# Optimization experiments

Hardware: AMD Instinct MI355X
Metric: run time of the kernel (lower is better)

Reference implementation:

```python
import jax, jax.numpy as jnp
import numpy as np
from math import factorial

# ---- static config (mirrors CACE_LR defaults) ----
MAX_L, MAX_NU = 3, 3
N_RBF, N_RADIAL = 6, 6
N_BASIS = 3                       # n_atom_basis
N_CH = N_BASIS * N_BASIS          # edge channels = 9
CUTOFF, P = 5.5, 6
NZ = 94                           # elements with Z < 95
N_NODES, N_EDGES, N_GRAPHS = 10000, 80000, 16
MP_NORM = 1.0 / np.sqrt(10.0)     # 1/sqrt(avg_num_neighbors)

# Cartesian angular monomials x^lx y^ly z^lz with lx+ly+lz = l <= MAX_L
LXLYLZ = [(lx, ly, l - lx - ly) for l in range(MAX_L + 1)
          for lx in range(l, -1, -1) for ly in range(l - lx, -1, -1)]
N_ANG = len(LXLYLZ)               # 20
MONO = np.array(LXLYLZ, np.int32)
L_OF = MONO.sum(1)                # l of each monomial
IDX000 = LXLYLZ.index((0, 0, 0))
MIDX = {m: i for i, m in enumerate(LXLYLZ)}

def _mult(m):
    return factorial(sum(m)) / (factorial(m[0]) * factorial(m[1]) * factorial(m[2]))

MULT = np.array([_mult(m) for m in LXLYLZ], np.float32)
# nu=2 invariants: per l>=1, sum_m mult(m) * A_m^2
NU2_W = [np.where(L_OF == l, MULT, 0.0).astype(np.float32) for l in range(1, MAX_L + 1)]
# nu=3 invariants: pairs (l1,l2), contract A_m1 * A_m2 * A_{m1+m2}
NU3 = []
for (l1, l2) in [(1, 1), (1, 2)]:
    i1s, i2s, i12s, cfs = [], [], [], []
    for m1 in [m for m in LXLYLZ if sum(m) == l1]:
        for m2 in [m for m in LXLYLZ if sum(m) == l2]:
            m12 = (m1[0] + m2[0], m1[1] + m2[1], m1[2] + m2[2])
            i1s.append(MIDX[m1]); i2s.append(MIDX[m2]); i12s.append(MIDX[m12])
            cfs.append(_mult(m12))
    NU3.append((np.array(i1s), np.array(i2s), np.array(i12s), np.array(cfs, np.float32)))
N_SYM = 1 + MAX_L + len(NU3)      # 6 symmetrized angular features
FLAT_DIM = N_RADIAL * N_SYM * N_CH * 2  # 648


def monomials(u):                 # u: [E,3] unit vectors -> [E, N_ANG]
    pows = jnp.stack([jnp.ones_like(u), u, u * u, u * u * u], axis=1)  # [E,4,3]
    return pows[:, MONO[:, 0], 0] * pows[:, MONO[:, 1], 1] * pows[:, MONO[:, 2], 2]


def symmetrize(A):                # A: [N,R,N_ANG,C] -> B: [N,R,N_SYM,C]
    outs = [A[:, :, IDX000, :]]
    A2 = A * A
    for w in NU2_W:
        outs.append(jnp.einsum('nrac,a->nrc', A2, jnp.asarray(w)))
    for i1, i2, i12, cf in NU3:
        outs.append(jnp.einsum('nrkc,k->nrc', A[:, :, i1] * A[:, :, i2] * A[:, :, i12],
                               jnp.asarray(cf)))
    return jnp.stack(outs, axis=2)


def radial_tf(A, W):              # shared-per-l radial linear, W: [MAX_L+1,R,S]
    return jnp.einsum('nrac,ars->nsac', A, W[L_OF])


def setup_inputs() -> dict:
    key = jax.random.key(0)
    ks = jax.random.split(key, 16)
    pos = jax.random.uniform(ks[0], (N_NODES, 3), jnp.float32) * 10.0  # 10 A box
    node_type = jax.random.randint(ks[1], (N_NODES,), 0, NZ)
    src = jax.random.randint(ks[2], (N_EDGES,), 0, N_NODES)
    dst = jax.random.randint(ks[3], (N_EDGES,), 0, N_NODES)
    shifts = jnp.zeros((N_EDGES, 3), jnp.float32)
    batch_ids = jnp.sort(jax.random.randint(ks[4], (N_NODES,), 0, N_GRAPHS))
    s = lambda k, sh, f: jax.random.normal(k, sh, jnp.float32) * f
    params = dict(
        Wemb=s(ks[5], (NZ, N_BASIS), 0.5),
        freqs=jnp.arange(1, N_RBF + 1, dtype=jnp.float32) * np.pi / CUTOFF,
        W_rt=s(ks[6], (MAX_L + 1, N_RBF, N_RADIAL), 1 / np.sqrt(N_RBF)),
        W_mem=s(ks[7], (MAX_L + 1, N_RADIAL, N_RADIAL), 1 / np.sqrt(N_RADIAL)),
        W_Ar=s(ks[8], (MAX_L + 1, N_RBF, N_RADIAL), 1 / np.sqrt(N_RBF)),
        W_chi=s(ks[9], (N_RADIAL * N_SYM * N_CH, N_CH), 1 / np.sqrt(N_RADIAL * N_SYM * N_CH)),
        W1=s(ks[10], (FLAT_DIM, 64), 1 / np.sqrt(FLAT_DIM)),
        b1=jnp.zeros((64,), jnp.float32),
        W2=s(ks[11], (64, 32), 1 / 8.0),
        b2=jnp.zeros((32,), jnp.float32),
        W3=s(ks[12], (32, 1), 1 / np.sqrt(32.0)),
        b3=jnp.zeros((1,), jnp.float32),
    )
    return dict(pos=pos, node_type=node_type, src=src, dst=dst,
                shifts=shifts, batch_ids=batch_ids, **params)


def reference(pos, node_type, src, dst, shifts, batch_ids, Wemb, freqs,
              W_rt, W_mem, W_Ar, W_chi, W1, b1, W2, b2, W3, b3):
    n = pos.shape[0]
    # edge geometry (get_edge_vectors_and_lengths, normalize=True)
    vec = pos[dst] - pos[src] + shifts
    r = jnp.linalg.norm(vec, axis=-1, keepdims=True) + 1e-9           # [E,1]
    unit = vec / r
    # Bessel RBF and polynomial cutoff (p=6)
    rbf = jnp.sqrt(2.0 / CUTOFF) * jnp.sin(r * freqs[None]) / r      # [E,R]
    u = r[:, 0] / CUTOFF
    fc = jnp.where(u < 1.0,
                   1.0 - (P + 1) * (P + 2) / 2.0 * u**P + P * (P + 2) * u**(P + 1)
                   - P * (P + 1) / 2.0 * u**(P + 2), 0.0)
    radial = rbf * fc[:, None]
    ang = monomials(unit)                                             # [E,N_ANG]
    # node one-hot + embedding folded into a table lookup; directed edge encoding
    emb = Wemb[node_type]                                             # [N,3]
    edge_code = (emb[src][:, :, None] * emb[dst][:, None, :]).reshape(-1, N_CH)
    # edge_attri[e,r,a,c] = radial * angular * edge_code
    edge_attri = radial[:, :, None, None] * ang[:, None, :, None] * edge_code[:, None, None, :]
    A = radial_tf(jax.ops.segment_sum(edge_attri, dst, num_segments=n), W_rt)
    B = symmetrize(A)
    B_list = [B]
    # ---- one message-passing step: M (memory) + Ar + Bchi ----
    memory = radial_tf(A, W_mem)
    chi = B.reshape(n, -1) @ W_chi                                    # [N,C]
    msg_B = edge_attri * chi[src][:, None, None, :]
    A_B = radial_tf(jax.ops.segment_sum(msg_B, dst, num_segments=n), W_rt)
    rad_Ar = jnp.einsum('er,ars->eas', rbf, W_Ar[L_OF]) * fc[:, None, None]  # [E,A,S]
    msg_Ar = A[src] * jnp.transpose(rad_Ar, (0, 2, 1))[:, :, :, None]
    A_r = jax.ops.segment_sum(msg_Ar, dst, num_segments=n)
    A = (A_r + A_B) * MP_NORM + memory
    B_list.append(symmetrize(A))
    feats = jnp.stack(B_list, axis=-1).reshape(n, -1)                 # [N, 648]
    # MLP readout (atomwise_hidden=[64,32], num_targets=1), SiLU activations
    h = jax.nn.silu(feats @ W1 + b1)
    h = jax.nn.silu(h @ W2 + b2)
    atomic = h @ W3 + b3                                              # [N,1]
    return jnp.squeeze(jax.ops.segment_sum(atomic, batch_ids, num_segments=N_GRAPHS))
```

## Files before the change

kernel.cpp:

```cpp
#include <hip/hip_runtime.h>
#include <hip/hip_bf16.h>
#include <math.h>

#define NE 80000
#define NN 10000
#define NG 16
#define NBLK 157
#define MP_NORM 0.31622776601683794f
#define RBF_NORM 0.60302268915552724f

__constant__ int c_mx[20] = {0, 1,0,0, 2,1,1,0,0,0, 3,2,2,1,1,1,0,0,0,0};
__constant__ int c_my[20] = {0, 0,1,0, 0,1,0,2,1,0, 0,1,0,2,1,0,3,2,1,0};
__constant__ int c_mz[20] = {0, 0,0,1, 0,0,1,0,1,2, 0,0,1,0,1,2,0,1,2,3};

__device__ __forceinline__ int l_of_a(int a) {
    return (a >= 10) ? 3 : ((a >= 4) ? 2 : ((a >= 1) ? 1 : 0));
}

__device__ __forceinline__ void symm_from_lds(const float* Als, float* brow,
                                              int lane) {
    if (lane >= 54) return;
    const int s2 = lane / 9, c = lane - s2 * 9;
    const float* a = Als + s2 * 180 + c;
    float v[20];
    #pragma unroll
    for (int i = 0; i < 20; i++) v[i] = a[i * 9];
    const float o0 = v[0];
    const float o1 = v[1]*v[1] + v[2]*v[2] + v[3]*v[3];
    const float o2 = v[4]*v[4] + 2.f*v[5]*v[5] + 2.f*v[6]*v[6]
                   + v[7]*v[7] + 2.f*v[8]*v[8] + v[9]*v[9];
    const float o3 = v[10]*v[10] + 3.f*v[11]*v[11] + 3.f*v[12]*v[12]
                   + 3.f*v[13]*v[13] + 6.f*v[14]*v[14] + 3.f*v[15]*v[15]
                   + v[16]*v[16] + 3.f*v[17]*v[17] + 3.f*v[18]*v[18] + v[19]*v[19];
    const float o4 = v[1]*v[1]*v[4] + 2.f*v[1]*v[2]*v[5] + 2.f*v[1]*v[3]*v[6]
                   + 2.f*v[2]*v[1]*v[5] + v[2]*v[2]*v[7] + 2.f*v[2]*v[3]*v[8]
                   + 2.f*v[3]*v[1]*v[6] + 2.f*v[3]*v[2]*v[8] + v[3]*v[3]*v[9];
    const float o5 =
        v[1]*(v[4]*v[10] + 3.f*v[5]*v[11] + 3.f*v[6]*v[12] + 3.f*v[7]*v[13]
              + 6.f*v[8]*v[14] + 3.f*v[9]*v[15])
      + v[2]*(3.f*v[4]*v[11] + 3.f*v[5]*v[13] + 6.f*v[6]*v[14] + v[7]*v[16]
              + 3.f*v[8]*v[17] + 3.f*v[9]*v[18])
      + v[3]*(3.f*v[4]*v[12] + 6.f*v[5]*v[14] + 3.f*v[6]*v[15] + 3.f*v[7]*v[17]
              + 3.f*v[8]*v[18] + v[9]*v[19]);
    float* b = brow + s2 * 54 + c;
    b[0]  = o0;
    b[9]  = o1;
    b[18] = o2;
    b[27] = o3;
    b[36] = o4;
    b[45] = o5;
}

__global__ __launch_bounds__(256) void k_hist(
    const float* __restrict__ pos, const int* __restrict__ src,
    const int* __restrict__ dst, const float* __restrict__ shifts,
    int* __restrict__ indeg)
{
    const int e = blockIdx.x * 256 + threadIdx.x;
    if (e >= NE) return;
    const int sn = src[e], dn = dst[e];
    const float vx = pos[3*dn+0] - pos[3*sn+0] + shifts[3*e+0];
    const float vy = pos[3*dn+1] - pos[3*sn+1] + shifts[3*e+1];
    const float vz = pos[3*dn+2] - pos[3*sn+2] + shifts[3*e+2];
    const float r = sqrtf(vx*vx + vy*vy + vz*vz) + 1e-9f;
    if (r * (1.0f / 5.5f) < 1.0f) atomicAdd(&indeg[dn], 1);
}

__global__ __launch_bounds__(256) void k_scan(const int* __restrict__ indeg,
                                              int* __restrict__ offs)
{
    __shared__ int part[256];
    const int t = threadIdx.x;
    int s = 0;
    for (int i = t * 40; i < t * 40 + 40; i++)
        if (i < NN) s += indeg[i];
    part[t] = s;
    __syncthreads();
    if (t == 0) {
        int run = 0;
        for (int i = 0; i < 256; i++) { int v = part[i]; part[i] = run; run += v; }
    }
    __syncthreads();
    int run = part[t];
    for (int i = t * 40; i < t * 40 + 40; i++) {
        if (i < NN) { offs[i] = run; run += indeg[i]; }
    }
}

__global__ __launch_bounds__(256) void k_fill(
    const float* __restrict__ pos, const int* __restrict__ src,
    const int* __restrict__ dst, const float* __restrict__ shifts,
    const int* __restrict__ ntype, const float* __restrict__ Wemb,
    const int* __restrict__ offs, int* __restrict__ cursor,
    int* __restrict__ esrc, float4* __restrict__ egeo,
    float* __restrict__ ecode)
{
    const int e = blockIdx.x * 256 + threadIdx.x;
    if (e >= NE) return;
    const int sn = src[e], dn = dst[e];
    const float vx = pos[3*dn+0] - pos[3*sn+0] + shifts[3*e+0];
    const float vy = pos[3*dn+1] - pos[3*sn+1] + shifts[3*e+1];
    const float vz = pos[3*dn+2] - pos[3*sn+2] + shifts[3*e+2];
    const float r = sqrtf(vx*vx + vy*vy + vz*vz) + 1e-9f;
    if (r * (1.0f / 5.5f) < 1.0f) {
        const int p = offs[dn] + atomicAdd(&cursor[dn], 1);
        esrc[p] = sn;
        const float inv = 1.0f / r;
        egeo[p] = make_float4(vx*inv, vy*inv, vz*inv, r);
        const int ts = ntype[sn], td = ntype[dn];
        const float es0 = Wemb[3*ts], es1 = Wemb[3*ts+1], es2 = Wemb[3*ts+2];
        const float ed0 = Wemb[3*td], ed1 = Wemb[3*td+1], ed2 = Wemb[3*td+2];
        float* cp = ecode + (size_t)p * 9;
        cp[0] = es0*ed0; cp[1] = es0*ed1; cp[2] = es0*ed2;
        cp[3] = es1*ed0; cp[4] = es1*ed1; cp[5] = es1*ed2;
        cp[6] = es2*ed0; cp[7] = es2*ed1; cp[8] = es2*ed2;
    }
}

__global__ __launch_bounds__(64) void k_node1(
    const float* __restrict__ freqs, const float* __restrict__ W_rt,
    const int* __restrict__ offs, const int* __restrict__ indeg,
    const int* __restrict__ esrc, const float4* __restrict__ egeo,
    const float* __restrict__ ecode, const float* __restrict__ W1,
    const float* __restrict__ W_chi,
    float* __restrict__ A, float* __restrict__ chi, float* __restrict__ P1)
{
    __shared__ float Als[1080];
    __shared__ float Bls[324];
    const int n = blockIdx.x, lane = threadIdx.x;
    int aslot[3], cslot[3], rslot[3];
    float acc[3][6];
    #pragma unroll
    for (int j = 0; j < 3; j++) {
        const int p = lane + 64 * j;
        const int pc = (p < 180) ? p : 0;
        aslot[j] = pc / 9;
        cslot[j] = 20 + pc % 9;
        rslot[j] = 29 + 6 * l_of_a(pc / 9);
        #pragma unroll
        for (int s = 0; s < 6; s++) acc[j][s] = 0.f;
    }
    float fr[6];
    #pragma unroll
    for (int q = 0; q < 6; q++) fr[q] = freqs[q];
    float wrt[6];
    if (lane >= 29 && lane < 53) {
        const int j = lane - 29, l = j / 6, s2 = j % 6;
        #pragma unroll
        for (int q = 0; q < 6; q++) wrt[q] = W_rt[(l*6 + q)*6 + s2];
    }
    int mlx = 0, mly = 0, mlz = 0;
    if (lane < 20) { mlx = c_mx[lane]; mly = c_my[lane]; mlz = c_mz[lane]; }
    const int e0 = offs[n], cnt = indeg[n];
    float4 geo = make_float4(0.f, 0.f, 0.f, 1.f);
    float ecd = 0.f;
    if (cnt > 0) {
        geo = egeo[e0];
        if (lane >= 20 && lane < 29) ecd = ecode[(size_t)e0*9 + lane - 20];
    }
    for (int t = 0; t < cnt; t++) {
        const float4 g = geo;
        const float ec = ecd;
        if (t + 1 < cnt) {
            geo = egeo[e0 + t + 1];
            if (lane >= 20 && lane < 29)
                ecd = ecode[(size_t)(e0 + t + 1)*9 + lane - 20];
        }
        float regX = ec;
        if (lane < 20) {
            float v = 1.f;
            for (int i = 0; i < mlx; i++) v *= g.x;
            for (int i = 0; i < mly; i++) v *= g.y;
            for (int i = 0; i < mlz; i++) v *= g.z;
            regX = v;
        } else if (lane >= 29 && lane < 53) {
            const float r = g.w;
            const float u = r * (1.0f / 5.5f);
            const float u2 = u*u, u3 = u2*u, u6 = u3*u3;
            const float fcv = 1.0f - 28.0f*u6 + 48.0f*u6*u - 21.0f*u6*u2;
            const float inv = fcv / r;
            float s = 0.f;
            #pragma unroll
            for (int q = 0; q < 6; q++)
                s += RBF_NORM * __sinf(r * fr[q]) * inv * wrt[q];
            regX = s;
        }
        float pp[3];
        #pragma unroll
        for (int j = 0; j < 3; j++)
            pp[j] = __shfl(regX, aslot[j]) * __shfl(regX, cslot[j]);
        #pragma unroll
        for (int j = 0; j < 3; j++) {
            #pragma unroll
            for (int s = 0; s < 6; s++)
                acc[j][s] = fmaf(__shfl(regX, rslot[j] + s), pp[j], acc[j][s]);
        }
    }
    #pragma unroll
    for (int j = 0; j < 3; j++) {
        const int p = lane + 64 * j;
        if (p < 180) {
            #pragma unroll
            for (int s = 0; s < 6; s++) {
                A[(size_t)n*1080 + s*180 + p] = acc[j][s];
                Als[s*180 + p] = acc[j][s];
            }
        }
    }
    __syncthreads();
    symm_from_lds(Als, Bls, lane);
    __syncthreads();
    {
        float s = 0.f;
        if (lane < 63) {
            const int cc = lane % 9, gg = lane / 9;
            const int jb = gg * 47;
            const int je = (jb + 47 < 324) ? (jb + 47) : 324;
            float wc = W_chi[jb * 9 + cc];
            for (int j = jb; j < je; j++) {
                const float wn = (j + 1 < je) ? W_chi[(j + 1) * 9 + cc] : 0.f;
                s = fmaf(Bls[j], wc, s);
                wc = wn;
            }
        }
        float tt;
        tt = __shfl(s, lane + 36); if (lane < 27) s += tt;
        tt = __shfl(s, lane + 18); if (lane < 18) s += tt;
        tt = __shfl(s, lane + 9);
        if (lane < 9) chi[(size_t)n * 9 + lane] = s + tt;
    }
    {
        float cur[6], nxt[6];
        #pragma unroll
        for (int u = 0; u < 6; u++) cur[u] = W1[(size_t)(2*u)*64 + lane];
        float s0=0.f, s1=0.f, s2=0.f, s3=0.f, s4=0.f, s5=0.f;
        for (int q = 0; q < 324; q += 6) {
            const int qn = q + 6;
            if (qn < 324) {
                #pragma unroll
                for (int u = 0; u < 6; u++)
                    nxt[u] = W1[(size_t)(2*(qn+u))*64 + lane];
            }
            s0 = fmaf(Bls[q+0], cur[0], s0);
            s1 = fmaf(Bls[q+1], cur[1], s1);
            s2 = fmaf(Bls[q+2], cur[2], s2);
            s3 = fmaf(Bls[q+3], cur[3], s3);
            s4 = fmaf(Bls[q+4], cur[4], s4);
            s5 = fmaf(Bls[q+5], cur[5], s5);
            #pragma unroll
            for (int u = 0; u < 6; u++) cur[u] = nxt[u];
        }
        P1[(size_t)n*64 + lane] = ((s0 + s1) + (s2 + s3)) + (s4 + s5);
    }
}

__global__ __launch_bounds__(64) void k_node2(
    const float* __restrict__ freqs, const float* __restrict__ W_rt,
    const float* __restrict__ W_Ar, const float* __restrict__ W_mem,
    const int* __restrict__ offs, const int* __restrict__ indeg,
    const int* __restrict__ esrc, const float4* __restrict__ egeo,
    const float* __restrict__ ecode, const float* __restrict__ chi,
    const float* __restrict__ A, const float* __restrict__ W1,
    float* __restrict__ P2)
{
    __shared__ float Als[1080];
    __shared__ float Qls[1080];
    __shared__ float Wm[144];
    __shared__ float B2ls[324];
    const int n = blockIdx.x, lane = threadIdx.x;
    #pragma unroll
    for (int k = 0; k < 17; k++) {
        const int i = lane + 64 * k;
        if (i < 1080) Als[i] = A[(size_t)n*1080 + i];
    }
    Wm[lane] = W_mem[lane];
    Wm[lane + 64] = W_mem[lane + 64];
    if (lane < 16) Wm[lane + 128] = W_mem[lane + 128];
    int aslot[3], cslot[3], rslot[3];
    float acc[3][6];
    #pragma unroll
    for (int j = 0; j < 3; j++) {
        const int p = lane + 64 * j;
        const int pc = (p < 180) ? p : 0;
        aslot[j] = pc / 9;
        cslot[j] = 20 + pc % 9;
        rslot[j] = 29 + 6 * l_of_a(pc / 9);
        #pragma unroll
        for (int s = 0; s < 6; s++) acc[j][s] = 0.f;
    }
    float fr[6];
    #pragma unroll
    for (int q = 0; q < 6; q++) fr[q] = freqs[q];
    float wrtB[6], wrtA[6];
    if (lane >= 29 && lane < 53) {
        const int j = lane - 29, l = j / 6, s2 = j % 6;
        #pragma unroll
        for (int q = 0; q < 6; q++) {
            wrtB[q] = W_rt[(l*6 + q)*6 + s2];
            wrtA[q] = W_Ar[(l*6 + q)*6 + s2];
        }
    }
    int mlx = 0, mly = 0, mlz = 0;
    if (lane < 20) { mlx = c_mx[lane]; mly = c_my[lane]; mlz = c_mz[lane]; }
    __syncthreads();
    const int e0 = offs[n], cnt = indeg[n];
    int sn2 = 0;
    float4 geo = make_float4(0.f, 0.f, 0.f, 1.f);
    float ecd = 0.f, chin = 0.f;
    float an[3][6];
    #pragma unroll
    for (int j = 0; j < 3; j++)
        #pragma unroll
        for (int s = 0; s < 6; s++) an[j][s] = 0.f;
    if (cnt > 0) {
        const int sn1 = esrc[e0];
        geo = egeo[e0];
        if (lane >= 20 && lane < 29) {
            ecd  = ecode[(size_t)e0*9 + lane - 20];
            chin = chi[(size_t)sn1*9 + lane - 20];
        }
        const float* ar = A + (size_t)sn1 * 1080;
        #pragma unroll
        for (int j = 0; j < 3; j++)
            #pragma unroll
            for (int s = 0; s < 6; s++) an[j][s] = ar[s*180 + lane + 64*j];
    }
    if (cnt > 1) sn2 = esrc[e0 + 1];
    for (int t = 0; t < cnt; t++) {
        const float4 g = geo;
        const float ec = ecd, ch = chin;
        float av[3][6];
        #pragma unroll
        for (int j = 0; j < 3; j++)
            #pragma unroll
            for (int s = 0; s < 6; s++) av[j][s] = an[j][s];
        if (t + 1 < cnt) {
            geo = egeo[e0 + t + 1];
            if (lane >= 20 && lane < 29) {
                ecd  = ecode[(size_t)(e0 + t + 1)*9 + lane - 20];
                chin = chi[(size_t)sn2*9 + lane - 20];
            }
            const float* ar = A + (size_t)sn2 * 1080;
            #pragma unroll
            for (int j = 0; j < 3; j++)
                #pragma unroll
                for (int s = 0; s < 6; s++) an[j][s] = ar[s*180 + lane + 64*j];
            if (t + 2 < cnt) sn2 = esrc[e0 + t + 2];
        }
        float regX = ec * ch;
        float regY = 0.f;
        if (lane < 20) {
            float v = 1.f;
            for (int i = 0; i < mlx; i++) v *= g.x;
            for (int i = 0; i < mly; i++) v *= g.y;
            for (int i = 0; i < mlz; i++) v *= g.z;
            regX = v;
        } else if (lane >= 29 && lane < 53) {
            const float r = g.w;
            const float u = r * (1.0f / 5.5f);
            const float u2 = u*u, u3 = u2*u, u6 = u3*u3;
            const float fcv = 1.0f - 28.0f*u6 + 48.0f*u6*u - 21.0f*u6*u2;
            const float inv = fcv / r;
            float sB = 0.f, sA = 0.f;
            #pragma unroll
            for (int q = 0; q < 6; q++) {
                const float rb = RBF_NORM * __sinf(r * fr[q]) * inv;
                sB = fmaf(rb, wrtB[q], sB);
                sA = fmaf(rb, wrtA[q], sA);
            }
            regX = sB;
            regY = sA;
        }
        float pp[3];
        #pragma unroll
        for (int j = 0; j < 3; j++)
            pp[j] = __shfl(regX, aslot[j]) * __shfl(regX, cslot[j]);
        #pragma unroll
        for (int j = 0; j < 3; j++) {
            #pragma unroll
            for (int s = 0; s < 6; s++) {
                const float rB = __shfl(regX, rslot[j] + s);
                const float rA = __shfl(regY, rslot[j] + s);
                acc[j][s] += rB * pp[j] + av[j][s] * rA;
            }
        }
    }
    #pragma unroll
    for (int j = 0; j < 3; j++) {
        const int p = lane + 64 * j;
        if (p < 180) {
            const int l = l_of_a(p / 9);
            float als6[6];
            #pragma unroll
            for (int sp = 0; sp < 6; sp++) als6[sp] = Als[sp*180 + p];
            #pragma unroll
            for (int s = 0; s < 6; s++) {
                float m = 0.f;
                #pragma unroll
                for (int sp = 0; sp < 6; sp++)
                    m = fmaf(als6[sp], Wm[l*36 + sp*6 + s], m);
                Qls[s*180 + p] = acc[j][s] * MP_NORM + m;
            }
        }
    }
    __syncthreads();
    symm_from_lds(Qls, B2ls, lane);
    __syncthreads();
    {
        float cur[6], nxt[6];
        #pragma unroll
        for (int u = 0; u < 6; u++) cur[u] = W1[(size_t)(2*u + 1)*64 + lane];
        float s0=0.f, s1=0.f, s2=0.f, s3=0.f, s4=0.f, s5=0.f;
        for (int q = 0; q < 324; q += 6) {
            const int qn = q + 6;
            if (qn < 324) {
                #pragma unroll
                for (int u = 0; u < 6; u++)
                    nxt[u] = W1[(size_t)(2*(qn+u) + 1)*64 + lane];
            }
            s0 = fmaf(B2ls[q+0], cur[0], s0);
            s1 = fmaf(B2ls[q+1], cur[1], s1);
            s2 = fmaf(B2ls[q+2], cur[2], s2);
            s3 = fmaf(B2ls[q+3], cur[3], s3);
            s4 = fmaf(B2ls[q+4], cur[4], s4);
            s5 = fmaf(B2ls[q+5], cur[5], s5);
            #pragma unroll
            for (int u = 0; u < 6; u++) cur[u] = nxt[u];
        }
        P2[(size_t)n*64 + lane] = ((s0 + s1) + (s2 + s3)) + (s4 + s5);
    }
}

__global__ __launch_bounds__(256) void k_tail(
    const float* __restrict__ P1, const float* __restrict__ P2,
    const float* __restrict__ b1, const float* __restrict__ W2,
    const float* __restrict__ b2, const float* __restrict__ W3,
    const float* __restrict__ b3, const int* __restrict__ batch,
    float* __restrict__ part)
{
    __shared__ float h1s[64][66];
    __shared__ float W2L[2048];
    __shared__ float gsum[16];
    const int tid = threadIdx.x;
    const int nb = blockIdx.x * 64;
    if (tid < 16) gsum[tid] = 0.f;
    for (int idx = tid; idx < 2048; idx += 256) W2L[idx] = W2[idx];
    for (int idx = tid; idx < 4096; idx += 256) {
        const int nl = idx >> 6, o = idx & 63;
        float h = 0.f;
        if (nb + nl < NN)
            h = P1[(size_t)(nb + nl)*64 + o] + P2[(size_t)(nb + nl)*64 + o]
              + b1[o];
        h1s[nl][o] = h / (1.f + __expf(-h));
    }
    __syncthreads();
    const int nl = tid >> 2, og = (tid & 3) * 8;
    float acc2[8];
    #pragma unroll
    for (int j = 0; j < 8; j++) acc2[j] = b2[og + j];
    #pragma unroll 8
    for (int k = 0; k < 64; k++) {
        const float hv = h1s[nl][k];
        const float4 wA = *(const float4*)&W2L[k*32 + og];
        const float4 wB = *(const float4*)&W2L[k*32 + og + 4];
        acc2[0] = fmaf(hv, wA.x, acc2[0]); acc2[1] = fmaf(hv, wA.y, acc2[1]);
        acc2[2] = fmaf(hv, wA.z, acc2[2]); acc2[3] = fmaf(hv, wA.w, acc2[3]);
        acc2[4] = fmaf(hv, wB.x, acc2[4]); acc2[5] = fmaf(hv, wB.y, acc2[5]);
        acc2[6] = fmaf(hv, wB.z, acc2[6]); acc2[7] = fmaf(hv, wB.w, acc2[7]);
    }
    float s = 0.f;
    #pragma unroll
    for (int j = 0; j < 8; j++) {
        const float g = acc2[j] / (1.f + __expf(-acc2[j]));
        s = fmaf(g, W3[og + j], s);
    }
    s += __shfl_xor(s, 1);
    s += __shfl_xor(s, 2);
    if ((tid & 3) == 0 && nb + nl < NN)
        atomicAdd(&gsum[batch[nb + nl]], s + b3[0]);
    __syncthreads();
    if (tid < 16) part[blockIdx.x * 16 + tid] = gsum[tid];
}

__global__ __launch_bounds__(64) void k_final(const float* __restrict__ part,
                                              float* __restrict__ out)
{
    const int t = threadIdx.x;
    if (t >= 16) return;
    float acc = 0.f;
    for (int b = 0; b < NBLK; b++) acc += part[b * 16 + t];
    out[t] = acc;
}

extern "C" void kernel_launch(void* const* d_in, const int* in_sizes, int n_in,
                              void* d_out, int out_size, void* d_ws, size_t ws_size,
                              hipStream_t stream)
{
    const float* pos    = (const float*)d_in[0];
    const int*   ntype  = (const int*)  d_in[1];
    const int*   src    = (const int*)  d_in[2];
    const int*   dst    = (const int*)  d_in[3];
    const float* shifts = (const float*)d_in[4];
    const int*   batch  = (const int*)  d_in[5];
    const float* Wemb   = (const float*)d_in[6];
    const float* freqs  = (const float*)d_in[7];
    const float* W_rt   = (const float*)d_in[8];
    const float* W_mem  = (const float*)d_in[9];
    const float* W_Ar   = (const float*)d_in[10];
    const float* W_chi  = (const float*)d_in[11];
    const float* W1     = (const float*)d_in[12];
    const float* b1     = (const float*)d_in[13];
    const float* W2     = (const float*)d_in[14];
    const float* b2     = (const float*)d_in[15];
    const float* W3     = (const float*)d_in[16];
    const float* b3     = (const float*)d_in[17];

    float*  ws    = (float*)d_ws;
    float*  A     = ws;
    float*  P1    = A    + (size_t)NN * 1080;
    float*  P2    = P1   + (size_t)NN * 64;
    float*  chi   = P2   + (size_t)NN * 64;
    float4* egeo  = (float4*)(chi + (size_t)NN * 9);
    int*    esrc  = (int*)(egeo + NE);
    float*  ecode = (float*)(esrc + NE);
    float*  part  = ecode + (size_t)NE * 9;
    int*    indeg  = (int*)(part + NBLK * 16);
    int*    offs   = indeg  + 10240;
    int*    cursor = offs   + 10240;

    hipMemsetAsync(indeg,  0, 10240 * sizeof(int), stream);
    hipMemsetAsync(cursor, 0, 10240 * sizeof(int), stream);

    k_hist<<<(NE + 255)/256, 256, 0, stream>>>(pos, src, dst, shifts, indeg);
    k_scan<<<1, 256, 0, stream>>>(indeg, offs);
    k_fill<<<(NE + 255)/256, 256, 0, stream>>>(pos, src, dst, shifts, ntype,
                                               Wemb, offs, cursor, esrc, egeo,
                                               ecode);
    k_node1<<<NN, 64, 0, stream>>>(freqs, W_rt, offs, indeg, esrc, egeo, ecode,
                                   W1, W_chi, A, chi, P1);
    k_node2<<<NN, 64, 0, stream>>>(freqs, W_rt, W_Ar, W_mem, offs, indeg, esrc,
                                   egeo, ecode, chi, A, W1, P2);
    k_tail<<<NBLK, 256, 0, stream>>>(P1, P2, b1, W2, b2, W3, b3, batch, part);
    k_final<<<1, 64, 0, stream>>>(part, (float*)d_out);
}
```

Baseline: 202.2 us.

## Split per-node edge loops across two wavefronts with LDS reduction

Both node kernels now run with 128 threads per block. Two wavefronts each take alternate incoming edges, and their partial accumulators are reduced through LDS. The radial coefficients are now broadcast through small LDS arrays with vector loads instead of many __shfl calls. The W1 projection is split in half across the two waves and then reduced. This is meant to shorten the serial per-edge chain and raise latency hiding, at the cost of extra LDS, extra barriers and idle lanes in the tail phases.

```diff
diff --git a/kernel.cpp b/kernel.cpp
--- a/kernel.cpp
+++ b/kernel.cpp
@@ -117,7 +117,7 @@
     }
 }
 
-__global__ __launch_bounds__(64) void k_node1(
+__global__ __launch_bounds__(128) void k_node1(
     const float* __restrict__ freqs, const float* __restrict__ W_rt,
     const int* __restrict__ offs, const int* __restrict__ indeg,
     const int* __restrict__ esrc, const float4* __restrict__ egeo,
@@ -126,9 +126,14 @@
     float* __restrict__ A, float* __restrict__ chi, float* __restrict__ P1)
 {
     __shared__ float Als[1080];
+    __shared__ float accW[1080];
     __shared__ float Bls[324];
-    const int n = blockIdx.x, lane = threadIdx.x;
-    int aslot[3], cslot[3], rslot[3];
+    __shared__ float red[64];
+    __shared__ float radLS[2][4][8];
+    const int tid = threadIdx.x;
+    const int lane = tid & 63, w = tid >> 6;
+    const int n = blockIdx.x;
+    int aslot[3], cslot[3], lofp[3];
     float acc[3][6];
     #pragma unroll
     for (int j = 0; j < 3; j++) {
@@ -136,7 +141,7 @@
         const int pc = (p < 180) ? p : 0;
         aslot[j] = pc / 9;
         cslot[j] = 20 + pc % 9;
-        rslot[j] = 29 + 6 * l_of_a(pc / 9);
+        lofp[j]  = l_of_a(pc / 9);
         #pragma unroll
         for (int s = 0; s < 6; s++) acc[j][s] = 0.f;
     }
@@ -154,17 +159,17 @@
     const int e0 = offs[n], cnt = indeg[n];
     float4 geo = make_float4(0.f, 0.f, 0.f, 1.f);
     float ecd = 0.f;
-    if (cnt > 0) {
-        geo = egeo[e0];
-        if (lane >= 20 && lane < 29) ecd = ecode[(size_t)e0*9 + lane - 20];
-    }
-    for (int t = 0; t < cnt; t++) {
+    if (w < cnt) {
+        geo = egeo[e0 + w];
+        if (lane >= 20 && lane < 29) ecd = ecode[(size_t)(e0 + w)*9 + lane - 20];
+    }
+    for (int t = w; t < cnt; t += 2) {
         const float4 g = geo;
         const float ec = ecd;
-        if (t + 1 < cnt) {
-            geo = egeo[e0 + t + 1];
+        if (t + 2 < cnt) {
+            geo = egeo[e0 + t + 2];
             if (lane >= 20 && lane < 29)
-                ecd = ecode[(size_t)(e0 + t + 1)*9 + lane - 20];
+                ecd = ecode[(size_t)(e0 + t + 2)*9 + lane - 20];
         }
         float regX = ec;
         if (lane < 20) {
@@ -183,7 +188,8 @@
             #pragma unroll
             for (int q = 0; q < 6; q++)
                 s += RBF_NORM * __sinf(r * fr[q]) * inv * wrt[q];
-            regX = s;
+            const int j = lane - 29;
+            radLS[w][j / 6][j % 6] = s;
         }
         float pp[3];
         #pragma unroll
@@ -191,26 +197,42 @@
             pp[j] = __shfl(regX, aslot[j]) * __shfl(regX, cslot[j]);
         #pragma unroll
         for (int j = 0; j < 3; j++) {
-            #pragma unroll
-            for (int s = 0; s < 6; s++)
-                acc[j][s] = fmaf(__shfl(regX, rslot[j] + s), pp[j], acc[j][s]);
-        }
-    }
-    #pragma unroll
-    for (int j = 0; j < 3; j++) {
-        const int p = lane + 64 * j;
-        if (p < 180) {
-            #pragma unroll
-            for (int s = 0; s < 6; s++) {
-                A[(size_t)n*1080 + s*180 + p] = acc[j][s];
-                Als[s*180 + p] = acc[j][s];
-            }
-        }
-    }
-    __syncthreads();
-    symm_from_lds(Als, Bls, lane);
-    __syncthreads();
-    {
+            const float* rp = &radLS[w][lofp[j]][0];
+            const float4 r4 = *(const float4*)rp;
+            const float2 r2 = *(const float2*)(rp + 4);
+            acc[j][0] = fmaf(r4.x, pp[j], acc[j][0]);
+            acc[j][1] = fmaf(r4.y, pp[j], acc[j][1]);
+            acc[j][2] = fmaf(r4.z, pp[j], acc[j][2]);
+            acc[j][3] = fmaf(r4.w, pp[j], acc[j][3]);
+            acc[j][4] = fmaf(r2.x, pp[j], acc[j][4]);
+            acc[j][5] = fmaf(r2.y, pp[j], acc[j][5]);
+        }
+    }
+    if (w == 1) {
+        #pragma unroll
+        for (int j = 0; j < 3; j++) {
+            const int p = lane + 64 * j;
+            if (p < 180)
+                #pragma unroll
+                for (int s = 0; s < 6; s++) accW[s*180 + p] = acc[j][s];
+        }
+    }
+    __syncthreads();
+    if (w == 0) {
+        #pragma unroll
+        for (int j = 0; j < 3; j++) {
+            const int p = lane + 64 * j;
+            if (p < 180)
+                #pragma unroll
+                for (int s = 0; s < 6; s++)
+                    Als[s*180 + p] = acc[j][s] + accW[s*180 + p];
+        }
+    }
+    __syncthreads();
+    for (int i = tid; i < 1080; i += 128) A[(size_t)n*1080 + i] = Als[i];
+    if (w == 0) symm_from_lds(Als, Bls, lane);
+    __syncthreads();
+    if (w == 1) {
         float s = 0.f;
         if (lane < 63) {
             const int cc = lane % 9, gg = lane / 9;
@@ -230,13 +252,14 @@
         if (lane < 9) chi[(size_t)n * 9 + lane] = s + tt;
     }
     {
+        const int qb = 162 * w;
         float cur[6], nxt[6];
         #pragma unroll
-        for (int u = 0; u < 6; u++) cur[u] = W1[(size_t)(2*u)*64 + lane];
+        for (int u = 0; u < 6; u++) cur[u] = W1[(size_t)(2*(qb+u))*64 + lane];
         float s0=0.f, s1=0.f, s2=0.f, s3=0.f, s4=0.f, s5=0.f;
-        for (int q = 0; q < 324; q += 6) {
+        for (int q = qb; q < qb + 162; q += 6) {
             const int qn = q + 6;
-            if (qn < 324) {
+            if (qn < qb + 162) {
                 #pragma unroll
                 for (int u = 0; u < 6; u++)
                     nxt[u] = W1[(size_t)(2*(qn+u))*64 + lane];
@@ -250,11 +273,14 @@
             #pragma unroll
             for (int u = 0; u < 6; u++) cur[u] = nxt[u];
         }
-        P1[(size_t)n*64 + lane] = ((s0 + s1) + (s2 + s3)) + (s4 + s5);
-    }
-}
-
-__global__ __launch_bounds__(64) void k_node2(
+        const float total = ((s0 + s1) + (s2 + s3)) + (s4 + s5);
+        if (w == 1) red[lane] = total;
+        __syncthreads();
+        if (w == 0) P1[(size_t)n*64 + lane] = total + red[lane];
+    }
+}
+
+__global__ __launch_bounds__(128) void k_node2(
     const float* __restrict__ freqs, const float* __restrict__ W_rt,
     const float* __restrict__ W_Ar, const float* __restrict__ W_mem,
     const int* __restrict__ offs, const int* __restrict__ indeg,
@@ -267,16 +293,15 @@
     __shared__ float Qls[1080];
     __shared__ float Wm[144];
     __shared__ float B2ls[324];
-    const int n = blockIdx.x, lane = threadIdx.x;
-    #pragma unroll
-    for (int k = 0; k < 17; k++) {
-        const int i = lane + 64 * k;
-        if (i < 1080) Als[i] = A[(size_t)n*1080 + i];
-    }
-    Wm[lane] = W_mem[lane];
-    Wm[lane + 64] = W_mem[lane + 64];
-    if (lane < 16) Wm[lane + 128] = W_mem[lane + 128];
-    int aslot[3], cslot[3], rslot[3];
+    __shared__ float red[64];
+    __shared__ float radB_LS[2][4][8];
+    __shared__ float radA_LS[2][4][8];
+    const int tid = threadIdx.x;
+    const int lane = tid & 63, w = tid >> 6;
+    const int n = blockIdx.x;
+    for (int i = tid; i < 1080; i += 128) Als[i] = A[(size_t)n*1080 + i];
+    for (int i = tid; i < 144; i += 128) Wm[i] = W_mem[i];
+    int aslot[3], cslot[3], lofp[3];
     float acc[3][6];
     #pragma unroll
     for (int j = 0; j < 3; j++) {
@@ -284,7 +309,7 @@
         const int pc = (p < 180) ? p : 0;
         aslot[j] = pc / 9;
         cslot[j] = 20 + pc % 9;
-        rslot[j] = 29 + 6 * l_of_a(pc / 9);
+        lofp[j]  = l_of_a(pc / 9);
         #pragma unroll
         for (int s = 0; s < 6; s++) acc[j][s] = 0.f;
     }
@@ -302,9 +327,8 @@
     }
     int mlx = 0, mly = 0, mlz = 0;
     if (lane < 20) { mlx = c_mx[lane]; mly = c_my[lane]; mlz = c_mz[lane]; }
-    __syncthreads();
     const int e0 = offs[n], cnt = indeg[n];
-    int sn2 = 0;
+    int snN = 0;
     float4 geo = make_float4(0.f, 0.f, 0.f, 1.f);
     float ecd = 0.f, chin = 0.f;
     float an[3][6];
@@ -312,21 +336,21 @@
     for (int j = 0; j < 3; j++)
         #pragma unroll
         for (int s = 0; s < 6; s++) an[j][s] = 0.f;
-    if (cnt > 0) {
-        const int sn1 = esrc[e0];
-        geo = egeo[e0];
+    if (w < cnt) {
+        const int s0 = esrc[e0 + w];
+        geo = egeo[e0 + w];
         if (lane >= 20 && lane < 29) {
-            ecd  = ecode[(size_t)e0*9 + lane - 20];
-            chin = chi[(size_t)sn1*9 + lane - 20];
-        }
-        const float* ar = A + (size_t)sn1 * 1080;
+            ecd  = ecode[(size_t)(e0 + w)*9 + lane - 20];
+            chin = chi[(size_t)s0*9 + lane - 20];
+        }
+        const float* ar = A + (size_t)s0 * 1080;
         #pragma unroll
         for (int j = 0; j < 3; j++)
             #pragma unroll
             for (int s = 0; s < 6; s++) an[j][s] = ar[s*180 + lane + 64*j];
     }
-    if (cnt > 1) sn2 = esrc[e0 + 1];
-    for (int t = 0; t < cnt; t++) {
+    if (w + 2 < cnt) snN = esrc[e0 + w + 2];
+    for (int t = w; t < cnt; t += 2) {
         const float4 g = geo;
         const float ec = ecd, ch = chin;
         float av[3][6];
@@ -334,21 +358,20 @@
         for (int j = 0; j < 3; j++)
             #pragma unroll
             for (int s = 0; s < 6; s++) av[j][s] = an[j][s];
-        if (t + 1 < cnt) {
-            geo = egeo[e0 + t + 1];
+        if (t + 2 < cnt) {
+            geo = egeo[e0 + t + 2];
             if (lane >= 20 && lane < 29) {
-                ecd  = ecode[(size_t)(e0 + t + 1)*9 + lane - 20];
-                chin = chi[(size_t)sn2*9 + lane - 20];
+                ecd  = ecode[(size_t)(e0 + t + 2)*9 + lane - 20];
+                chin = chi[(size_t)snN*9 + lane - 20];
             }
-            const float* ar = A + (size_t)sn2 * 1080;
+            const float* ar = A + (size_t)snN * 1080;
             #pragma unroll
             for (int j = 0; j < 3; j++)
                 #pragma unroll
                 for (int s = 0; s < 6; s++) an[j][s] = ar[s*180 + lane + 64*j];
-            if (t + 2 < cnt) sn2 = esrc[e0 + t + 2];
+            if (t + 4 < cnt) snN = esrc[e0 + t + 4];
         }
         float regX = ec * ch;
-        float regY = 0.f;
         if (lane < 20) {
             float v = 1.f;
             for (int i = 0; i < mlx; i++) v *= g.x;
@@ -368,8 +391,9 @@
                 sB = fmaf(rb, wrtB[q], sB);
                 sA = fmaf(rb, wrtA[q], sA);
             }
-            regX = sB;
-            regY = sA;
+            const int j = lane - 29;
+            radB_LS[w][j / 6][j % 6] = sB;
+            radA_LS[w][j / 6][j % 6] = sA;
         }
         float pp[3];
         #pragma unroll
@@ -377,43 +401,67 @@
             pp[j] = __shfl(regX, aslot[j]) * __shfl(regX, cslot[j]);
         #pragma unroll
         for (int j = 0; j < 3; j++) {
-            #pragma unroll
-            for (int s = 0; s < 6; s++) {
-                const float rB = __shfl(regX, rslot[j] + s);
-                const float rA = __shfl(regY, rslot[j] + s);
-                acc[j][s] += rB * pp[j] + av[j][s] * rA;
-            }
-        }
-    }
-    #pragma unroll
-    for (int j = 0; j < 3; j++) {
-        const int p = lane + 64 * j;
-        if (p < 180) {
-            const int l = l_of_a(p / 9);
-            float als6[6];
-            #pragma unroll
-            for (int sp = 0; sp < 6; sp++) als6[sp] = Als[sp*180 + p];
-            #pragma unroll
-            for (int s = 0; s < 6; s++) {
-                float m = 0.f;
-                #pragma unroll
-                for (int sp = 0; sp < 6; sp++)
-                    m = fmaf(als6[sp], Wm[l*36 + sp*6 + s], m);
-                Qls[s*180 + p] = acc[j][s] * MP_NORM + m;
-            }
-        }
-    }
-    __syncthreads();
-    symm_from_lds(Qls, B2ls, lane);
+            const float* rbp = &radB_LS[w][lofp[j]][0];
+            const float* rap = &radA_LS[w][lofp[j]][0];
+            const float4 b4 = *(const float4*)rbp;
+            const float2 b2 = *(const float2*)(rbp + 4);
+            const float4 a4 = *(const float4*)rap;
+            const float2 a2 = *(const float2*)(rap + 4);
+            acc[j][0] += b4.x * pp[j] + av[j][0] * a4.x;
+            acc[j][1] += b4.y * pp[j] + av[j][1] * a4.y;
+            acc[j][2] += b4.z * pp[j] + av[j][2] * a4.z;
+            acc[j][3] += b4.w * pp[j] + av[j][3] * a4.w;
+            acc[j][4] += b2.x * pp[j] + av[j][4] * a2.x;
+            acc[j][5] += b2.y * pp[j] + av[j][5] * a2.y;
+        }
+    }
+    if (w == 1) {
+        #pragma unroll
+        for (int j = 0; j < 3; j++) {
+            const int p = lane + 64 * j;
+            if (p < 180)
+                #pragma unroll
+                for (int s = 0; s < 6; s++) Qls[s*180 + p] = acc[j][s];
+        }
+    }
+    __syncthreads();
+    if (w == 0) {
+        #pragma unroll
+        for (int j = 0; j < 3; j++) {
+            const int p = lane + 64 * j;
+            if (p < 180)
+                #pragma unroll
+                for (int s = 0; s < 6; s++) Qls[s*180 + p] += acc[j][s];
+        }
+    }
+    __syncthreads();
+    for (int p = tid; p < 180; p += 128) {
+        const int l = l_of_a(p / 9);
+        float als6[6];
+        #pragma unroll
+        for (int sp = 0; sp < 6; sp++) als6[sp] = Als[sp*180 + p];
+        #pragma unroll
+        for (int s = 0; s < 6; s++) {
+            float m = 0.f;
+            #pragma unroll
+            for (int sp = 0; sp < 6; sp++)
+                m = fmaf(als6[sp], Wm[l*36 + sp*6 + s], m);
+            Qls[s*180 + p] = Qls[s*180 + p] * MP_NORM + m;
+        }
+    }
+    __syncthreads();
+    if (w == 0) symm_from_lds(Qls, B2ls, lane);
     __syncthreads();
     {
+        const int qb = 162 * w;
         float cur[6], nxt[6];
         #pragma unroll
-        for (int u = 0; u < 6; u++) cur[u] = W1[(size_t)(2*u + 1)*64 + lane];
+        for (int u = 0; u < 6; u++)
+            cur[u] = W1[(size_t)(2*(qb+u) + 1)*64 + lane];
         float s0=0.f, s1=0.f, s2=0.f, s3=0.f, s4=0.f, s5=0.f;
-        for (int q = 0; q < 324; q += 6) {
+        for (int q = qb; q < qb + 162; q += 6) {
             const int qn = q + 6;
-            if (qn < 324) {
+            if (qn < qb + 162) {
                 #pragma unroll
                 for (int u = 0; u < 6; u++)
                     nxt[u] = W1[(size_t)(2*(qn+u) + 1)*64 + lane];
@@ -427,7 +475,10 @@
             #pragma unroll
             for (int u = 0; u < 6; u++) cur[u] = nxt[u];
         }
-        P2[(size_t)n*64 + lane] = ((s0 + s1) + (s2 + s3)) + (s4 + s5);
+        const float total = ((s0 + s1) + (s2 + s3)) + (s4 + s5);
+        if (w == 1) red[lane] = total;
+        __syncthreads();
+        if (w == 0) P2[(size_t)n*64 + lane] = total + red[lane];
     }
 }
 
@@ -536,10 +587,10 @@
     k_fill<<<(NE + 255)/256, 256, 0, stream>>>(pos, src, dst, shifts, ntype,
                                                Wemb, offs, cursor, esrc, egeo,
                                                ecode);
-    k_node1<<<NN, 64, 0, stream>>>(freqs, W_rt, offs, indeg, esrc, egeo, ecode,
-                                   W1, W_chi, A, chi, P1);
-    k_node2<<<NN, 64, 0, stream>>>(freqs, W_rt, W_Ar, W_mem, offs, indeg, esrc,
-                                   egeo, ecode, chi, A, W1, P2);
+    k_node1<<<NN, 128, 0, stream>>>(freqs, W_rt, offs, indeg, esrc, egeo, ecode,
+                                    W1, W_chi, A, chi, P1);
+    k_node2<<<NN, 128, 0, stream>>>(freqs, W_rt, W_Ar, W_mem, offs, indeg, esrc,
+                                    egeo, ecode, chi, A, W1, P2);
     k_tail<<<NBLK, 256, 0, stream>>>(P1, P2, b1, W2, b2, W3, b3, batch, part);
     k_final<<<1, 64, 0, stream>>>(part, (float*)d_out);
 }
```

Result: slower. 207.9 us (+2.8%).
